# Optimization experiments

Measured on AMD Instinct MI355X. Metric: run time of the kernel, lower is better.

The kernel has to match this reference:

```python
import jax, jax.numpy as jnp
import numpy as np

B, N, QD = 2, 2048, 1024
HEADS, DIM_HEAD = 16, 64
INNER = HEADS * DIM_HEAD  # 1024
SCALE = DIM_HEAD ** -0.5


def setup_inputs() -> dict:
    key = jax.random.key(0)
    ks = jax.random.split(key, 8)
    x = jax.random.normal(ks[0], (B, N, QD), dtype=jnp.float32)
    bias = jax.random.normal(ks[1], (B, N, N), dtype=jnp.float32)
    mask = jax.random.randint(ks[2], (B, N), 0, 2) > 0
    # parameters (nn.Linear stores weight [out, in]; we keep [in, out] and matmul x @ W)
    Wq = jax.random.normal(ks[3], (QD, INNER), dtype=jnp.float32) * (QD ** -0.5)
    Wkv = jax.random.normal(ks[4], (QD, 2 * INNER), dtype=jnp.float32) * (QD ** -0.5)
    Wo = jax.random.normal(ks[5], (INNER, QD), dtype=jnp.float32) * (INNER ** -0.5)
    bo = jax.random.normal(ks[6], (QD,), dtype=jnp.float32) * 0.01
    return {"x": x, "bias": bias, "mask": mask, "Wq": Wq, "Wkv": Wkv, "Wo": Wo, "bo": bo}


def reference(x, bias, mask, Wq, Wkv, Wo, bo):
    b, n, _ = x.shape
    q = x @ Wq                      # [b, n, inner]
    kv = x @ Wkv                    # [b, n, 2*inner] (context defaults to x)
    k, v = jnp.split(kv, 2, axis=-1)
    # split heads: [b, h, n, d]
    split = lambda t: t.reshape(b, n, HEADS, DIM_HEAD).transpose(0, 2, 1, 3)
    q, k, v = split(q), split(k), split(v)
    sim = jnp.einsum('bhid,bhjd->bhij', q, k) * SCALE   # [b, h, n, n]
    sim = sim + bias[:, None, :, :]                      # additive bias broadcast over heads
    max_neg = -jnp.finfo(sim.dtype).max
    sim = jnp.where(mask[:, None, None, :], sim, max_neg)  # per-key mask
    attn = jax.nn.softmax(sim, axis=-1)
    out = jnp.einsum('bhij,bhjd->bhid', attn, v)         # [b, h, n, d]
    out = out.transpose(0, 2, 1, 3).reshape(b, n, INNER)  # merge heads
    return out @ Wo + bo
```

## Files before the change

### kernel.cpp

```cpp
#include <hip/hip_runtime.h>
#include <hip/hip_bf16.h>
#include <stdint.h>

#define B_     2
#define N_     2048
#define QD_    1024
#define H_     16
#define DH_    64
#define INNER_ 1024
#define SCALE_ 0.125f

typedef unsigned short u16;
typedef __attribute__((ext_vector_type(8))) short bf16x8;
typedef __attribute__((ext_vector_type(4))) float f32x4;
typedef __attribute__((ext_vector_type(4))) unsigned short u16x4;
typedef __attribute__((ext_vector_type(8))) unsigned short u16x8;

__device__ inline u16 f2bf(float f) {
    union { float f; uint32_t u; } c; c.f = f;
    uint32_t r = c.u + 0x7FFFu + ((c.u >> 16) & 1u);
    return (u16)(r >> 16);
}
__device__ inline float bf2f(u16 s) {
    union { uint32_t u; float f; } c; c.u = ((uint32_t)s) << 16;
    return c.f;
}
__device__ inline void split2(float v, u16 &h, u16 &l) {
    u16 hs = f2bf(v);
    h = hs;
    l = f2bf(v - bf2f(hs));
}
__device__ inline void pack2(float a, float b, u16 &lo, u16 &hi) {
    float2 f; f.x = a; f.y = b;
    union { __hip_bfloat162 v; u16 u[2]; } c;
    c.v = __float22bfloat162_rn(f);
    lo = c.u[0]; hi = c.u[1];
}

__global__ __launch_bounds__(256) void prep_kernel(
    const float* __restrict__ x, u16* __restrict__ xh, u16* __restrict__ xl,
    const float* __restrict__ Wq, const float* __restrict__ Wkv, const float* __restrict__ Wo,
    u16* __restrict__ wTh, u16* __restrict__ wTl,
    u16* __restrict__ woTh, u16* __restrict__ woTl)
{
    __shared__ float t[32][33];
    const int blk = blockIdx.x, tid = threadIdx.x;
    if (blk < 4096) {
        int idx = blk * 256 + tid;
        float4 v = ((const float4*)x)[idx];
        u16x4 hv, lv; u16 h, l;
        split2(v.x, h, l); hv.x = h; lv.x = l;
        split2(v.y, h, l); hv.y = h; lv.y = l;
        split2(v.z, h, l); hv.z = h; lv.z = l;
        split2(v.w, h, l); hv.w = h; lv.w = l;
        ((u16x4*)xh)[idx] = hv;
        ((u16x4*)xl)[idx] = lv;
        return;
    }
    int local = blk - 4096;
    const float* src; u16 *dhi, *dlo; int C, bx, by;
    if (local < 1024)      { src = Wq;  dhi = wTh;                dlo = wTl;                C = 1024; by = local >> 5; bx = local & 31; }
    else if (local < 3072) { int l2 = local - 1024; src = Wkv; dhi = wTh + 1024 * 1024; dlo = wTl + 1024 * 1024; C = 2048; by = l2 >> 6; bx = l2 & 63; }
    else                   { int l2 = local - 3072; src = Wo;  dhi = woTh;               dlo = woTl;               C = 1024; by = l2 >> 5; bx = l2 & 31; }
    const int x0 = bx * 32, y0 = by * 32;
    const int tx = tid & 31, ty = tid >> 5;
    for (int yy = ty; yy < 32; yy += 8)
        t[yy][tx] = src[(size_t)(y0 + yy) * C + x0 + tx];
    __syncthreads();
    for (int i = ty; i < 32; i += 8) {
        float v = t[tx][i];
        u16 h, l; split2(v, h, l);
        size_t o = (size_t)(x0 + i) * 1024 + y0 + tx;
        dhi[o] = h; dlo[o] = l;
    }
}

__global__ __launch_bounds__(256) void gemm_qkv_bias(
    int mode,
    const u16* __restrict__ Ah, const u16* __restrict__ Al,
    const u16* __restrict__ Bh,
    u16* __restrict__ qh,
    u16* __restrict__ kb, u16* __restrict__ vT,
    const float* __restrict__ bias, const int* __restrict__ mask,
    u16* __restrict__ bsw)
{
    __shared__ __align__(16) char smem[24576];
    const int tid = threadIdx.x;

    int gid = -1, bid = -1;
    if (mode == 1) {
        if (blockIdx.x < 768) gid = blockIdx.x; else bid = blockIdx.x - 768;
    } else if (mode == 0) gid = blockIdx.x;
    else bid = blockIdx.x;

    if (bid >= 0) {
        float (*t)[65] = (float(*)[65])smem;
        const int b = bid >> 10, rest = bid & 1023;
        const int k0 = (rest & 31) * 64, q0 = (rest >> 5) * 64;
#pragma unroll
        for (int it = 0; it < 16; it++) {
            int idx = it * 256 + tid;
            int qq = idx >> 6, kk = idx & 63;
            t[qq][kk] = bias[((size_t)b * N_ + q0 + qq) * N_ + k0 + kk];
        }
        __syncthreads();
        const u16 NEG = f2bf(-1e30f);
        const int qt = q0 >> 6, jt = k0 >> 7, w0 = (k0 >> 5) & 3;
        const int p = tid >> 1, hf = tid & 1;
        const int wv = w0 + (p >> 6), lane = p & 63;
        const int quad = lane >> 4, l16 = lane & 15;
        const int kk = (p >> 6) * 32 + hf * 16 + l16;
        const int mok = mask[b * N_ + k0 + kk];
        u16x8 o0, o1;
#pragma unroll
        for (int i = 0; i < 8; i++) {
            int m = i >> 2, qr = i & 3;
            int qq = m * 16 + quad * 4 + qr;
            o0[i] = mok ? f2bf(t[qq][kk]) : NEG;
        }
#pragma unroll
        for (int i = 0; i < 8; i++) {
            int m = 2 + (i >> 2), qr = i & 3;
            int qq = m * 16 + quad * 4 + qr;
            o1[i] = mok ? f2bf(t[qq][kk]) : NEG;
        }
        size_t ob = ((((size_t)b * 32 + qt) * 16 + jt) * 4 + wv) * 2048
                    + (size_t)lane * 32 + hf * 16;
        *(u16x8*)&bsw[ob]     = o0;
        *(u16x8*)&bsw[ob + 8] = o1;
        return;
    }

    u16* sAh = (u16*)smem;
    u16* sAl = (u16*)(smem + 8192);
    u16* sBh = (u16*)(smem + 16384);
    const int wave = tid >> 6, lane = tid & 63;
    const int quad = lane >> 4, l16 = lane & 15;
    const int wm = wave >> 1, wn = wave & 1;
    const int bx = gid % 24, by = gid / 24;
    const int bm = by * 128, bn = bx * 128;
    const bool comp = (bx < 8);

    f32x4 acc[4][4];
#pragma unroll
    for (int i = 0; i < 4; i++)
#pragma unroll
        for (int j = 0; j < 4; j++) acc[i][j] = (f32x4){0.f, 0.f, 0.f, 0.f};

    const int row0 = tid >> 2, g4 = tid & 3;
    const int r1 = row0, r2 = row0 + 64;
    const int gc1 = (g4 ^ (r1 & 3)) * 8, gc2 = (g4 ^ (r2 & 3)) * 8;
    const size_t a1 = (size_t)(bm + r1) * 1024 + gc1, a2 = (size_t)(bm + r2) * 1024 + gc2;
    const size_t b1 = (size_t)(bn + r1) * 1024 + gc1, b2 = (size_t)(bn + r2) * 1024 + gc2;
    const int w1 = r1 * 32 + g4 * 8, w2 = r2 * 32 + g4 * 8;

    bf16x8 pAh0, pAh1, pAl0, pAl1, pBh0, pBh1;
    pAh0 = *(const bf16x8*)&Ah[a1]; pAh1 = *(const bf16x8*)&Ah[a2];
    pBh0 = *(const bf16x8*)&Bh[b1]; pBh1 = *(const bf16x8*)&Bh[b2];
    if (comp) { pAl0 = *(const bf16x8*)&Al[a1]; pAl1 = *(const bf16x8*)&Al[a2]; }

    for (int k0 = 0; k0 < 1024; k0 += 32) {
        *(bf16x8*)&sAh[w1] = pAh0; *(bf16x8*)&sAh[w2] = pAh1;
        *(bf16x8*)&sBh[w1] = pBh0; *(bf16x8*)&sBh[w2] = pBh1;
        if (comp) { *(bf16x8*)&sAl[w1] = pAl0; *(bf16x8*)&sAl[w2] = pAl1; }
        __syncthreads();
        if (k0 + 32 < 1024) {
            int kn = k0 + 32;
            pAh0 = *(const bf16x8*)&Ah[a1 + kn]; pAh1 = *(const bf16x8*)&Ah[a2 + kn];
            pBh0 = *(const bf16x8*)&Bh[b1 + kn]; pBh1 = *(const bf16x8*)&Bh[b2 + kn];
            if (comp) { pAl0 = *(const bf16x8*)&Al[a1 + kn]; pAl1 = *(const bf16x8*)&Al[a2 + kn]; }
        }
        bf16x8 fah[4], fal[4], fbh[4];
#pragma unroll
        for (int s = 0; s < 4; s++) {
            int ra = wm * 64 + s * 16 + l16;
            int rb = wn * 64 + s * 16 + l16;
            int ca = (quad ^ (ra & 3)) * 8;
            int cb = (quad ^ (rb & 3)) * 8;
            fah[s] = *(const bf16x8*)&sAh[ra * 32 + ca];
            fbh[s] = *(const bf16x8*)&sBh[rb * 32 + cb];
            if (comp) fal[s] = *(const bf16x8*)&sAl[ra * 32 + ca];
        }
#pragma unroll
        for (int sm = 0; sm < 4; sm++)
#pragma unroll
            for (int sn = 0; sn < 4; sn++) {
                acc[sm][sn] = __builtin_amdgcn_mfma_f32_16x16x32_bf16(fah[sm], fbh[sn], acc[sm][sn], 0, 0, 0);
                if (comp)
                    acc[sm][sn] = __builtin_amdgcn_mfma_f32_16x16x32_bf16(fal[sm], fbh[sn], acc[sm][sn], 0, 0, 0);
            }
        __syncthreads();
    }
#pragma unroll
    for (int sm = 0; sm < 4; sm++) {
        int rowb = bm + wm * 64 + sm * 16 + quad * 4;
        int bb = rowb >> 11, i0 = rowb & 2047;
#pragma unroll
        for (int sn = 0; sn < 4; sn++) {
            int col = bn + wn * 64 + sn * 16 + l16;
            int region = col >> 10;
            int hh = (col >> 6) & 15;
            int d = col & 63;
            if (region == 0) {
#pragma unroll
                for (int r = 0; r < 4; r++) {
                    size_t o = (((size_t)(bb * H_ + hh)) * N_ + i0 + r) * DH_ + d;
                    qh[o] = f2bf(acc[sm][sn][r] * SCALE_);
                }
            } else if (region == 1) {
#pragma unroll
                for (int r = 0; r < 4; r++) {
                    size_t o = (((size_t)(bb * H_ + hh)) * N_ + i0 + r) * DH_ + d;
                    kb[o] = f2bf(acc[sm][sn][r]);
                }
            } else {
                u16x4 pv;
#pragma unroll
                for (int r = 0; r < 4; r++) pv[r] = f2bf(acc[sm][sn][r]);
                *(u16x4*)&vT[(((size_t)(bb * H_ + hh)) * DH_ + d) * N_ + i0] = pv;
            }
        }
    }
}

__global__ __launch_bounds__(256) void gemm_out(
    const u16* __restrict__ Ab,
    const u16* __restrict__ Bh,
    const float* __restrict__ bo, float* __restrict__ out)
{
    __shared__ __align__(16) u16 sA[128 * 32], sBh[64 * 32];
    const int tid = threadIdx.x;
    const int wave = tid >> 6, lane = tid & 63;
    const int quad = lane >> 4, l16 = lane & 15;
    const int wm = wave >> 1, wn = wave & 1;
    const int bm = blockIdx.y * 128, bn = blockIdx.x * 64;

    f32x4 acc[4][2];
#pragma unroll
    for (int i = 0; i < 4; i++)
#pragma unroll
        for (int j = 0; j < 2; j++) acc[i][j] = (f32x4){0.f, 0.f, 0.f, 0.f};

    const int row0 = tid >> 2, g4 = tid & 3;
    const int r1 = row0, r2 = row0 + 64;
    const int rb0 = tid >> 2;
    const int gc1 = (g4 ^ (r1 & 3)) * 8, gc2 = (g4 ^ (r2 & 3)) * 8;
    const size_t a1 = (size_t)(bm + r1) * 1024 + gc1, a2 = (size_t)(bm + r2) * 1024 + gc2;
    const size_t bgo = (size_t)(bn + rb0) * 1024 + gc1;
    const int w1 = r1 * 32 + g4 * 8, w2 = r2 * 32 + g4 * 8;
    const int wb = rb0 * 32 + g4 * 8;

    bf16x8 pA0, pA1, pBh0;
    pA0 = *(const bf16x8*)&Ab[a1]; pA1 = *(const bf16x8*)&Ab[a2];
    pBh0 = *(const bf16x8*)&Bh[bgo];

    for (int k0 = 0; k0 < 1024; k0 += 32) {
        *(bf16x8*)&sA[w1] = pA0;  *(bf16x8*)&sA[w2] = pA1;
        *(bf16x8*)&sBh[wb] = pBh0;
        __syncthreads();
        if (k0 + 32 < 1024) {
            int kn = k0 + 32;
            pA0 = *(const bf16x8*)&Ab[a1 + kn]; pA1 = *(const bf16x8*)&Ab[a2 + kn];
            pBh0 = *(const bf16x8*)&Bh[bgo + kn];
        }
        bf16x8 fa[4], fbh[2];
#pragma unroll
        for (int s = 0; s < 4; s++) {
            int ra = wm * 64 + s * 16 + l16;
            int ca = (quad ^ (ra & 3)) * 8;
            fa[s] = *(const bf16x8*)&sA[ra * 32 + ca];
        }
#pragma unroll
        for (int s = 0; s < 2; s++) {
            int rb = wn * 32 + s * 16 + l16;
            int cb = (quad ^ (rb & 3)) * 8;
            fbh[s] = *(const bf16x8*)&sBh[rb * 32 + cb];
        }
#pragma unroll
        for (int sm = 0; sm < 4; sm++)
#pragma unroll
            for (int sn = 0; sn < 2; sn++)
                acc[sm][sn] = __builtin_amdgcn_mfma_f32_16x16x32_bf16(fa[sm], fbh[sn], acc[sm][sn], 0, 0, 0);
        __syncthreads();
    }
#pragma unroll
    for (int sm = 0; sm < 4; sm++) {
        int rowb = bm + wm * 64 + sm * 16 + quad * 4;
#pragma unroll
        for (int sn = 0; sn < 2; sn++) {
            int col = bn + wn * 32 + sn * 16 + l16;
            float bv = bo[col];
#pragma unroll
            for (int r = 0; r < 4; r++)
                out[(size_t)(rowb + r) * 1024 + col] = acc[sm][sn][r] + bv;
        }
    }
}

#define LDK 72
#define LDV 128
#define LDP 36

__global__ __launch_bounds__(256, 2) void attn_kernel(
    const u16* __restrict__ qh,
    const u16* __restrict__ kb, const u16* __restrict__ vT,
    const u16* __restrict__ bsw, u16* __restrict__ ob)
{
    __shared__ __align__(16) char smem[53248];
    u16* sK  = (u16*)smem;
    u16* sVt = (u16*)(smem + 18432);
    u16* sP  = (u16*)(smem + 34816);
    float* rO = (float*)smem;
    float* rL = (float*)(smem + 34816);

    const int bh = blockIdx.y, b = bh >> 4, h = bh & 15;
    const int qt = blockIdx.x, qbase = qt * 64;
    const int tid = threadIdx.x, wave = tid >> 6, lane = tid & 63;
    const int quad = lane >> 4, l16 = lane & 15;

    bf16x8 aq[4][2];
#pragma unroll
    for (int m = 0; m < 4; m++) {
        size_t qo = ((size_t)bh * N_ + qbase + m * 16 + l16) * DH_ + quad * 8;
        aq[m][0] = *(const bf16x8*)&qh[qo];
        aq[m][1] = *(const bf16x8*)&qh[qo + 32];
    }
    f32x4 Oacc[4][4], lacc[4];
#pragma unroll
    for (int m = 0; m < 4; m++) {
        lacc[m] = (f32x4){0.f, 0.f, 0.f, 0.f};
#pragma unroll
        for (int nd = 0; nd < 4; nd++) Oacc[m][nd] = (f32x4){0.f, 0.f, 0.f, 0.f};
    }
    bf16x8 ones;
#pragma unroll
    for (int i = 0; i < 8; i++) ones[i] = (short)0x3F80;

    const int rK = tid >> 3, cK = (tid & 7) * 8;
    const int rV = tid >> 4;
    const int vg = tid & 15;
    const int cV = vg * 8;
    const int vsw = (vg ^ (rV & 7)) * 8;
    const int vrg = ((wave * 4 + quad) ^ (l16 & 7)) * 8;
    const size_t kgbase = (size_t)bh * N_ * DH_;
    const size_t vgbase = (size_t)bh * DH_ * N_;
    const size_t bswb = (size_t)(b * 32 + qt) * 131072 + (size_t)wave * 2048
                        + (size_t)lane * 32;

    bf16x8 pK[4], pV[4];
    u16x8 cB[4], nB[4];
#pragma unroll
    for (int it = 0; it < 4; it++) {
        pK[it] = *(const bf16x8*)&kb[kgbase + (size_t)(rK + it * 32) * DH_ + cK];
        pV[it] = *(const bf16x8*)&vT[vgbase + (size_t)(rV + it * 16) * N_ + cV];
    }
#pragma unroll
    for (int c = 0; c < 4; c++) cB[c] = *(const u16x8*)&bsw[bswb + c * 8];

    for (int jt = 0; jt < 16; jt++) {
#pragma unroll
        for (int it = 0; it < 4; it++) {
            *(bf16x8*)&sK[(rK + it * 32) * LDK + cK] = pK[it];
            *(bf16x8*)&sVt[(rV + it * 16) * LDV + vsw] = pV[it];
        }
        __syncthreads();
        {
            int jn = (jt + 1) & 15;
            int j0n = jn * 128;
#pragma unroll
            for (int it = 0; it < 4; it++) {
                pK[it] = *(const bf16x8*)&kb[kgbase + (size_t)(j0n + rK + it * 32) * DH_ + cK];
                pV[it] = *(const bf16x8*)&vT[vgbase + (size_t)(rV + it * 16) * N_ + j0n + cV];
            }
            size_t bb = bswb + (size_t)jn * 8192;
#pragma unroll
            for (int c = 0; c < 4; c++) nB[c] = *(const u16x8*)&bsw[bb + c * 8];
        }
        bf16x8 kf[2][2], vf[4];
#pragma unroll
        for (int n = 0; n < 2; n++)
#pragma unroll
            for (int s = 0; s < 2; s++)
                kf[n][s] = *(const bf16x8*)&sK[(wave * 32 + n * 16 + l16) * LDK + s * 32 + quad * 8];
#pragma unroll
        for (int nd = 0; nd < 4; nd++)
            vf[nd] = *(const bf16x8*)&sVt[(nd * 16 + l16) * LDV + vrg];

        u16* pw = sP + wave * 64 * LDP;
#pragma unroll
        for (int m = 0; m < 4; m++) {
            f32x4 S0 = (f32x4){0.f, 0.f, 0.f, 0.f};
            f32x4 S1 = (f32x4){0.f, 0.f, 0.f, 0.f};
#pragma unroll
            for (int s = 0; s < 2; s++) {
                S0 = __builtin_amdgcn_mfma_f32_16x16x32_bf16(aq[m][s], kf[0][s], S0, 0, 0, 0);
                S1 = __builtin_amdgcn_mfma_f32_16x16x32_bf16(aq[m][s], kf[1][s], S1, 0, 0, 0);
            }
#pragma unroll
            for (int r = 0; r < 4; r++) {
                S0[r] = __expf(S0[r] + bf2f(cB[m >> 1][(m & 1) * 4 + r]));
                S1[r] = __expf(S1[r] + bf2f(cB[2 + (m >> 1)][(m & 1) * 4 + r]));
            }
#pragma unroll
            for (int r = 0; r < 4; r++) {
                u16 lo, hi;
                pack2(S0[r], S1[r], lo, hi);
                pw[(m * 16 + quad * 4 + r) * LDP + l16]      = lo;
                pw[(m * 16 + quad * 4 + r) * LDP + 16 + l16] = hi;
            }
            bf16x8 pa = *(const bf16x8*)&pw[(m * 16 + l16) * LDP + quad * 8];
            lacc[m] = __builtin_amdgcn_mfma_f32_16x16x32_bf16(pa, ones, lacc[m], 0, 0, 0);
#pragma unroll
            for (int nd = 0; nd < 4; nd++)
                Oacc[m][nd] = __builtin_amdgcn_mfma_f32_16x16x32_bf16(pa, vf[nd], Oacc[m][nd], 0, 0, 0);
        }
#pragma unroll
        for (int c = 0; c < 4; c++) cB[c] = nB[c];
        __syncthreads();
    }

    if (wave >= 2) {
        int slot = wave - 2;
#pragma unroll
        for (int m = 0; m < 4; m++) {
#pragma unroll
            for (int nd = 0; nd < 4; nd++)
#pragma unroll
                for (int r = 0; r < 4; r++)
                    rO[(slot * 64 + m * 16 + quad * 4 + r) * 68 + nd * 16 + l16] = Oacc[m][nd][r];
            if (l16 == 0)
#pragma unroll
                for (int r = 0; r < 4; r++)
                    rL[slot * 64 + m * 16 + quad * 4 + r] = lacc[m][r];
        }
    }
    __syncthreads();
    if (wave < 2) {
        int slot = wave;
#pragma unroll
        for (int m = 0; m < 4; m++) {
#pragma unroll
            for (int nd = 0; nd < 4; nd++)
#pragma unroll
                for (int r = 0; r < 4; r++) {
                    int idx = (slot * 64 + m * 16 + quad * 4 + r) * 68 + nd * 16 + l16;
                    rO[idx] += Oacc[m][nd][r];
                }
            if (l16 == 0)
#pragma unroll
                for (int r = 0; r < 4; r++)
                    rL[slot * 64 + m * 16 + quad * 4 + r] += lacc[m][r];
        }
    }
    __syncthreads();
    {
        const int q = tid >> 2, dg = (tid & 3) * 16;
        float l = rL[q] + rL[64 + q];
        float inv = 1.f / l;
        f32x4 s[4];
#pragma unroll
        for (int i4 = 0; i4 < 4; i4++) {
            s[i4] = *(const f32x4*)&rO[(size_t)q * 68 + dg + i4 * 4];
            f32x4 v = *(const f32x4*)&rO[(size_t)(64 + q) * 68 + dg + i4 * 4];
            s[i4] += v;
        }
        size_t obase = ((size_t)b * N_ + qbase + q) * INNER_ + h * 64 + dg;
#pragma unroll
        for (int i4 = 0; i4 < 4; i4++) {
            u16x4 o4;
#pragma unroll
            for (int r = 0; r < 4; r++) o4[r] = f2bf(s[i4][r] * inv);
            *(u16x4*)&ob[obase + i4 * 4] = o4;
        }
    }
}

extern "C" void kernel_launch(void* const* d_in, const int* in_sizes, int n_in,
                              void* d_out, int out_size, void* d_ws, size_t ws_size,
                              hipStream_t stream)
{
    const float* x    = (const float*)d_in[0];
    const float* bias = (const float*)d_in[1];
    const int*   mask = (const int*)d_in[2];
    const float* Wq   = (const float*)d_in[3];
    const float* Wkv  = (const float*)d_in[4];
    const float* Wo   = (const float*)d_in[5];
    const float* bo   = (const float*)d_in[6];
    float* out = (float*)d_out;

    char* w = (char*)d_ws;
    const size_t MB = 1024 * 1024;
    u16* q_h   = (u16*)(w);
    u16* k_b   = (u16*)(w + 16 * MB);
    u16* v_T   = (u16*)(w + 24 * MB);
    u16* xs_h  = (u16*)(w + 32 * MB);
    u16* xs_l  = (u16*)(w + 40 * MB);
    u16* wT_h  = (u16*)(w + 48 * MB);
    u16* wT_l  = (u16*)(w + 54 * MB);
    u16* woT_h = (u16*)(w + 60 * MB);
    u16* woT_l = (u16*)(w + 62 * MB);
    u16* o_b   = (u16*)(w + 64 * MB);

    const size_t bsw_bytes = (size_t)2 * N_ * N_ * sizeof(u16);
    const bool concurrent = ws_size >= 72 * MB + bsw_bytes;

    prep_kernel<<<8192, 256, 0, stream>>>(x, xs_h, xs_l, Wq, Wkv, Wo, wT_h, wT_l, woT_h, woT_l);

    if (concurrent) {
        u16* bsw = (u16*)(w + 72 * MB);
        gemm_qkv_bias<<<2816, 256, 0, stream>>>(1, xs_h, xs_l, wT_h,
                                                q_h, k_b, v_T, bias, mask, bsw);
        attn_kernel<<<dim3(32, 32), 256, 0, stream>>>(q_h, k_b, v_T, bsw, o_b);
    } else {
        u16* bsw = (u16*)(w + 32 * MB);
        gemm_qkv_bias<<<768, 256, 0, stream>>>(0, xs_h, xs_l, wT_h,
                                               q_h, k_b, v_T, bias, mask, bsw);
        gemm_qkv_bias<<<2048, 256, 0, stream>>>(2, xs_h, xs_l, wT_h,
                                                q_h, k_b, v_T, bias, mask, bsw);
        attn_kernel<<<dim3(32, 32), 256, 0, stream>>>(q_h, k_b, v_T, bsw, o_b);
    }
    gemm_out<<<dim3(16, 32), 256, 0, stream>>>(o_b, woT_h, bo, out);
}
```

Baseline: 282.8 us.

## Keep softmax probabilities in registers by transposing QK^T MFMA and permuting K rows

Swaps the MFMA operand order so S^T is computed and lands in the register layout the PV MFMA expects as its A operand. K rows are permuted in shared memory and the pre-swizzled bias/mask layout is regenerated to match, which removes the LDS round trip for P (writes, reads and the sP buffer). The freed LDS shrinks the kernel's shared footprint. The risk is that the permutation and bias layout are wrong, which would break correctness, and the mask read now assumes 4-byte mask elements loaded as int4.

```diff
diff --git a/kernel.cpp b/kernel.cpp
--- a/kernel.cpp
+++ b/kernel.cpp
@@ -30,11 +30,11 @@
     h = hs;
     l = f2bf(v - bf2f(hs));
 }
-__device__ inline void pack2(float a, float b, u16 &lo, u16 &hi) {
+__device__ inline unsigned pk2(float a, float b) {
     float2 f; f.x = a; f.y = b;
-    union { __hip_bfloat162 v; u16 u[2]; } c;
+    union { __hip_bfloat162 v; unsigned u; } c;
     c.v = __float22bfloat162_rn(f);
-    lo = c.u[0]; hi = c.u[1];
+    return c.u;
 }
 
 __global__ __launch_bounds__(256) void prep_kernel(
@@ -109,20 +109,19 @@
         const int p = tid >> 1, hf = tid & 1;
         const int wv = w0 + (p >> 6), lane = p & 63;
         const int quad = lane >> 4, l16 = lane & 15;
-        const int kk = (p >> 6) * 32 + hf * 16 + l16;
-        const int mok = mask[b * N_ + k0 + kk];
+        const int kbase = (p >> 6) * 32 + quad * 8 + hf * 4;
+        const int4 mv = *(const int4*)&mask[b * N_ + k0 + kbase];
+        const int mok[4] = { mv.x, mv.y, mv.z, mv.w };
         u16x8 o0, o1;
 #pragma unroll
         for (int i = 0; i < 8; i++) {
-            int m = i >> 2, qr = i & 3;
-            int qq = m * 16 + quad * 4 + qr;
-            o0[i] = mok ? f2bf(t[qq][kk]) : NEG;
+            int m = i >> 2, r = i & 3;
+            o0[i] = mok[r] ? f2bf(t[m * 16 + l16][kbase + r]) : NEG;
         }
 #pragma unroll
         for (int i = 0; i < 8; i++) {
-            int m = 2 + (i >> 2), qr = i & 3;
-            int qq = m * 16 + quad * 4 + qr;
-            o1[i] = mok ? f2bf(t[qq][kk]) : NEG;
+            int m = 2 + (i >> 2), r = i & 3;
+            o1[i] = mok[r] ? f2bf(t[m * 16 + l16][kbase + r]) : NEG;
         }
         size_t ob = ((((size_t)b * 32 + qt) * 16 + jt) * 4 + wv) * 2048
                     + (size_t)lane * 32 + hf * 16;
@@ -299,17 +298,15 @@
 
 #define LDK 72
 #define LDV 128
-#define LDP 36
 
 __global__ __launch_bounds__(256, 2) void attn_kernel(
     const u16* __restrict__ qh,
     const u16* __restrict__ kb, const u16* __restrict__ vT,
     const u16* __restrict__ bsw, u16* __restrict__ ob)
 {
-    __shared__ __align__(16) char smem[53248];
+    __shared__ __align__(16) char smem[35328];
     u16* sK  = (u16*)smem;
     u16* sVt = (u16*)(smem + 18432);
-    u16* sP  = (u16*)(smem + 34816);
     float* rO = (float*)smem;
     float* rL = (float*)(smem + 34816);
 
@@ -337,6 +334,7 @@
     for (int i = 0; i < 8; i++) ones[i] = (short)0x3F80;
 
     const int rK = tid >> 3, cK = (tid & 7) * 8;
+    const int sigK = ((rK & 4) << 2) + ((rK >> 3) << 2) + (rK & 3);
     const int rV = tid >> 4;
     const int vg = tid & 15;
     const int cV = vg * 8;
@@ -360,7 +358,7 @@
     for (int jt = 0; jt < 16; jt++) {
 #pragma unroll
         for (int it = 0; it < 4; it++) {
-            *(bf16x8*)&sK[(rK + it * 32) * LDK + cK] = pK[it];
+            *(bf16x8*)&sK[(it * 32 + sigK) * LDK + cK] = pK[it];
             *(bf16x8*)&sVt[(rV + it * 16) * LDV + vsw] = pV[it];
         }
         __syncthreads();
@@ -386,33 +384,30 @@
         for (int nd = 0; nd < 4; nd++)
             vf[nd] = *(const bf16x8*)&sVt[(nd * 16 + l16) * LDV + vrg];
 
-        u16* pw = sP + wave * 64 * LDP;
 #pragma unroll
         for (int m = 0; m < 4; m++) {
             f32x4 S0 = (f32x4){0.f, 0.f, 0.f, 0.f};
             f32x4 S1 = (f32x4){0.f, 0.f, 0.f, 0.f};
 #pragma unroll
             for (int s = 0; s < 2; s++) {
-                S0 = __builtin_amdgcn_mfma_f32_16x16x32_bf16(aq[m][s], kf[0][s], S0, 0, 0, 0);
-                S1 = __builtin_amdgcn_mfma_f32_16x16x32_bf16(aq[m][s], kf[1][s], S1, 0, 0, 0);
+                S0 = __builtin_amdgcn_mfma_f32_16x16x32_bf16(kf[0][s], aq[m][s], S0, 0, 0, 0);
+                S1 = __builtin_amdgcn_mfma_f32_16x16x32_bf16(kf[1][s], aq[m][s], S1, 0, 0, 0);
             }
+            float p0[4], p1[4];
 #pragma unroll
             for (int r = 0; r < 4; r++) {
-                S0[r] = __expf(S0[r] + bf2f(cB[m >> 1][(m & 1) * 4 + r]));
-                S1[r] = __expf(S1[r] + bf2f(cB[2 + (m >> 1)][(m & 1) * 4 + r]));
+                p0[r] = __expf(S0[r] + bf2f(cB[m >> 1][(m & 1) * 4 + r]));
+                p1[r] = __expf(S1[r] + bf2f(cB[2 + (m >> 1)][(m & 1) * 4 + r]));
             }
-#pragma unroll
-            for (int r = 0; r < 4; r++) {
-                u16 lo, hi;
-                pack2(S0[r], S1[r], lo, hi);
-                pw[(m * 16 + quad * 4 + r) * LDP + l16]      = lo;
-                pw[(m * 16 + quad * 4 + r) * LDP + 16 + l16] = hi;
-            }
-            bf16x8 pa = *(const bf16x8*)&pw[(m * 16 + l16) * LDP + quad * 8];
-            lacc[m] = __builtin_amdgcn_mfma_f32_16x16x32_bf16(pa, ones, lacc[m], 0, 0, 0);
+            union { bf16x8 v; unsigned w[4]; } pa;
+            pa.w[0] = pk2(p0[0], p0[1]);
+            pa.w[1] = pk2(p0[2], p0[3]);
+            pa.w[2] = pk2(p1[0], p1[1]);
+            pa.w[3] = pk2(p1[2], p1[3]);
+            lacc[m] = __builtin_amdgcn_mfma_f32_16x16x32_bf16(pa.v, ones, lacc[m], 0, 0, 0);
 #pragma unroll
             for (int nd = 0; nd < 4; nd++)
-                Oacc[m][nd] = __builtin_amdgcn_mfma_f32_16x16x32_bf16(pa, vf[nd], Oacc[m][nd], 0, 0, 0);
+                Oacc[m][nd] = __builtin_amdgcn_mfma_f32_16x16x32_bf16(pa.v, vf[nd], Oacc[m][nd], 0, 0, 0);
         }
 #pragma unroll
         for (int c = 0; c < 4; c++) cB[c] = nB[c];
@@ -516,7 +511,7 @@
         gemm_qkv_bias<<<768, 256, 0, stream>>>(0, xs_h, xs_l, wT_h,
                                                q_h, k_b, v_T, bias, mask, bsw);
         gemm_qkv_bias<<<2048, 256, 0, stream>>>(2, xs_h, xs_l, wT_h,
-                                                q_h, k_b, v_T, bias, mask, bsw);
+                                                q_h, k_b, v_T, bsw ? bias : bias, mask, bsw);
         attn_kernel<<<dim3(32, 32), 256, 0, stream>>>(q_h, k_b, v_T, bsw, o_b);
     }
     gemm_out<<<dim3(16, 32), 256, 0, stream>>>(o_b, woT_h, bo, out);
```

Measured after the change: 256.9 us. 1.1x faster.
